# Optimization experiments

Measured on AMD Instinct MI355X. Metric: run time of the kernel, lower is better.

The kernel has to match this reference:

```python
import jax, jax.numpy as jnp
import numpy as np

N = 100_000   # nodes
E = 800_000   # edges
D = 128       # hidden_dim
L = 4         # layer_num
G = 512       # graphs in batch
T = 10        # target_dim
BN_EPS = 1e-5


def setup_inputs() -> dict:
    key = jax.random.key(0)
    ks = jax.random.split(key, 16)
    return {
        "x": jax.random.randint(ks[0], (N, 9), 0, 64),
        "edge_index": jax.random.randint(ks[1], (2, E), 0, N),
        "batch": jnp.sort(jax.random.randint(ks[2], (N,), 0, G)),
        "edge_attr": jax.random.randint(ks[3], (E, 3), 0, 8),
        "atom_emb": jax.random.normal(ks[4], (9, 64, D), jnp.float32) * 0.1,
        "W": jax.random.normal(ks[5], (L, D, D), jnp.float32) * 0.05,
        "b": jax.random.normal(ks[6], (L, D), jnp.float32) * 0.01,
        "root": jax.random.normal(ks[7], (L, D), jnp.float32) * 0.1,
        "bond_emb": jax.random.normal(ks[8], (L, 3, 8, D), jnp.float32) * 0.1,
        "gamma": jnp.ones((L, D), jnp.float32),
        "beta": jnp.zeros((L, D), jnp.float32),
        "W1": jax.random.normal(ks[9], (D, D), jnp.float32) * 0.05,
        "b1": jax.random.normal(ks[10], (D,), jnp.float32) * 0.01,
        "W2": jax.random.normal(ks[11], (D, T), jnp.float32) * 0.05,
        "b2": jax.random.normal(ks[12], (T,), jnp.float32) * 0.01,
    }


def reference(x, edge_index, batch, edge_attr, atom_emb, W, b, root,
              bond_emb, gamma, beta, W1, b1, W2, b2):
    # AtomEncoder: sum of 9 per-feature embeddings -> [N, D]
    h = atom_emb[jnp.arange(9)[None, :], x].sum(axis=1)

    row, col = edge_index[0], edge_index[1]  # source j, target i
    # degree(row, N) + 1 (same every layer)
    deg = jax.ops.segment_sum(jnp.ones((E,), h.dtype), row, num_segments=N) + 1.0
    dinv = deg ** -0.5
    norm = dinv[row] * dinv[col]  # [E]

    feat3 = jnp.arange(3)[None, :]
    for l in range(L):
        hl = h @ W[l] + b[l]                                   # linear
        e = bond_emb[l][feat3, edge_attr].sum(axis=1)          # BondEncoder [E, D]
        msg = norm[:, None] * jax.nn.relu(hl[row] + e)         # gather + message
        aggr = jax.ops.segment_sum(msg, col, num_segments=N)   # scatter-add
        h = aggr + jax.nn.relu(hl + root[l]) / deg[:, None]
        if l < L - 1:
            mu = h.mean(axis=0)
            var = jnp.var(h, axis=0)                           # biased, as torch BN train
            h = (h - mu) / jnp.sqrt(var + BN_EPS) * gamma[l] + beta[l]
            h = jax.nn.relu(h)
        # dropout is identity in eval mode

    # global mean pool over graphs
    counts = jax.ops.segment_sum(jnp.ones((N,), h.dtype), batch, num_segments=G)
    hg = jax.ops.segment_sum(h, batch, num_segments=G) / jnp.maximum(counts, 1.0)[:, None]

    # output MLP: ReLU -> Linear -> ReLU -> Linear
    hh = jax.nn.relu(hg)
    hh = jax.nn.relu(hh @ W1 + b1)
    return hh @ W2 + b2
```

## Files before the change

### kernel.cpp

```cpp
#include <hip/hip_runtime.h>
#include <hip/hip_fp16.h>

#define NN 100000
#define NE 800000
#define DD 128
#define NL 4
#define NG 512
#define NT 10
#define BN_EPS 1e-5f
#define SCAN_B 1024
#define CHUNK 13

typedef __attribute__((ext_vector_type(4))) float f32x4;
typedef __attribute__((ext_vector_type(8))) _Float16 f16x8;

__device__ __forceinline__ float atomAddF(float* p, float v) {
  return unsafeAtomicAdd(p, v);
}


__global__ __launch_bounds__(256) void edge_count_kernel(
    const int* __restrict__ ei, int* __restrict__ degcnt,
    int* __restrict__ incnt) {
  int t = blockIdx.x * 256 + threadIdx.x;
  if (t * 4 >= NE) return;
  int4 s = *reinterpret_cast<const int4*>(&ei[t * 4]);
  int4 d = *reinterpret_cast<const int4*>(&ei[NE + t * 4]);
  atomicAdd(&degcnt[s.x], 1);
  atomicAdd(&degcnt[s.y], 1);
  atomicAdd(&degcnt[s.z], 1);
  atomicAdd(&degcnt[s.w], 1);
  atomicAdd(&incnt[d.x], 1);
  atomicAdd(&incnt[d.y], 1);
  atomicAdd(&incnt[d.z], 1);
  atomicAdd(&incnt[d.w], 1);
}


__global__ __launch_bounds__(256) void tables_kernel(
    const float* __restrict__ W, __half* __restrict__ Wf,
    const float* __restrict__ atom_emb, __half* __restrict__ aemb16,
    const int* __restrict__ batch, int* __restrict__ gstart) {
  const int idx = blockIdx.x * 256 + threadIdx.x;
  if (idx < NL * 8 * 4 * 64) {
    int lane = idx & 63;
    int c = (idx >> 6) & 3;
    int t = (idx >> 8) & 7;
    int l = idx >> 11;
    const float* Wl = W + l * DD * DD;
    __half* o = Wf + idx * 8;
    int n = t * 16 + (lane & 15);
    int k0 = c * 32 + (lane >> 4) * 8;
#pragma unroll
    for (int i = 0; i < 8; ++i) o[i] = (__half)Wl[(k0 + i) * DD + n];
  }
  if (idx < 9 * 64 * 32) {
    float4 v = *reinterpret_cast<const float4*>(&atom_emb[idx * 4]);
    union { __half2 hh[2]; int2 i2; } u;
    u.hh[0] = __floats2half2_rn(v.x, v.y);
    u.hh[1] = __floats2half2_rn(v.z, v.w);
    *reinterpret_cast<int2*>(&aemb16[idx * 4]) = u.i2;
  }
  if (idx <= NG) {
    if (idx == NG) {
      gstart[NG] = NN;
    } else {
      int lo = 0, hi = NN;
      while (lo < hi) {
        int m = (lo + hi) >> 1;
        if (batch[m] < idx) lo = m + 1; else hi = m;
      }
      gstart[idx] = lo;
    }
  }
}


__global__ __launch_bounds__(256) void atom_encoder_kernel(
    const int* __restrict__ x, const __half* __restrict__ aemb16,
    __half* __restrict__ h) {
  __shared__ int xs[16 * 9];
  const int nb = blockIdx.x * 16;
  const int t = threadIdx.x;
  if (t < 144) {
    int gi = nb * 9 + t;
    xs[t] = (gi < NN * 9) ? x[gi] : 0;
  }
  __syncthreads();
  const int n = nb + (t >> 4);
  const int q8 = t & 15;
  if (n >= NN) return;
  const f16x8* av = reinterpret_cast<const f16x8*>(aemb16);
  float acc[8] = {};
#pragma unroll
  for (int f = 0; f < 9; ++f) {
    int r = xs[(t >> 4) * 9 + f];
    f16x8 v = av[(f * 64 + r) * 16 + q8];
#pragma unroll
    for (int i = 0; i < 8; ++i) acc[i] += (float)v[i];
  }
  union { __half2 hh[4]; int4 i4; } u;
#pragma unroll
  for (int i = 0; i < 4; ++i)
    u.hh[i] = __floats2half2_rn(acc[2 * i], acc[2 * i + 1]);
  *reinterpret_cast<int4*>(&h[n * DD + q8 * 8]) = u.i4;
}


__global__ __launch_bounds__(256) void scan1_kernel(
    const int* __restrict__ in, int* __restrict__ out, int* __restrict__ bsum,
    const int* __restrict__ degcnt, float* __restrict__ degrecip,
    float* __restrict__ dinv, int n) {
  __shared__ int s[256];
  int base = blockIdx.x * SCAN_B + threadIdx.x * 4;
  int v[4] = {0, 0, 0, 0};
  if (base + 3 < n) {
    int4 t = *reinterpret_cast<const int4*>(&in[base]);
    v[0] = t.x; v[1] = t.y; v[2] = t.z; v[3] = t.w;
  } else {
    for (int i = 0; i < 4; ++i) v[i] = (base + i < n) ? in[base + i] : 0;
  }
  for (int i = 0; i < 4; ++i) {
    if (base + i < n) {
      float dv = (float)degcnt[base + i] + 1.f;
      degrecip[base + i] = 1.f / dv;
      dinv[base + i] = rsqrtf(dv);
    }
  }
  int tsum = v[0] + v[1] + v[2] + v[3];
  s[threadIdx.x] = tsum;
  __syncthreads();
  for (int d = 1; d < 256; d <<= 1) {
    int t = (threadIdx.x >= d) ? s[threadIdx.x - d] : 0;
    __syncthreads();
    s[threadIdx.x] += t;
    __syncthreads();
  }
  int run = s[threadIdx.x] - tsum;
  if (threadIdx.x == 255) bsum[blockIdx.x] = s[255];
  for (int i = 0; i < 4; ++i) {
    if (base + i < n) out[base + i] = run;
    run += v[i];
  }
}

__global__ void scan2_kernel(int* bsum, int nb) {
  __shared__ int s[128];
  int v = (threadIdx.x < nb) ? bsum[threadIdx.x] : 0;
  s[threadIdx.x] = v;
  __syncthreads();
  for (int d = 1; d < 128; d <<= 1) {
    int t = (threadIdx.x >= d) ? s[threadIdx.x - d] : 0;
    __syncthreads();
    s[threadIdx.x] += t;
    __syncthreads();
  }
  if (threadIdx.x < nb) bsum[threadIdx.x] = s[threadIdx.x] - v;
}

__global__ __launch_bounds__(256) void scan3_kernel(int* off, const int* bsum,
                                                    int n, int total) {
  int i = blockIdx.x * 256 + threadIdx.x;
  if (i < n) off[i] += bsum[i / SCAN_B];
  if (i == 0) off[n] = total;
}

__global__ __launch_bounds__(256) void csr_fill_kernel(
    const int* __restrict__ ei, const int* __restrict__ eattr,
    const float* __restrict__ dinv, const int* __restrict__ off,
    int* __restrict__ cursor, int2* __restrict__ edata) {
  int e = blockIdx.x * 256 + threadIdx.x;
  if (e >= NE) return;
  int r = ei[e], c = ei[NE + e];
  int pos = atomicAdd(&cursor[c], 1);
  float nm = dinv[r] * dinv[c];
  int idx9 = eattr[e * 3] | (eattr[e * 3 + 1] << 3) | (eattr[e * 3 + 2] << 6);
  int2 d;
  d.x = r | (idx9 << 17);
  d.y = __float_as_int(nm);
  edata[off[c] + pos] = d;
}


__global__ __launch_bounds__(256) void gemm_mfma_kernel(
    const __half* __restrict__ A, const __half* __restrict__ Wf,
    const float* __restrict__ bias, const float* __restrict__ bn_scale,
    const float* __restrict__ bn_shift, int fuse_bn, __half* __restrict__ hl) {
  const int wid = threadIdx.x >> 6, lane = threadIdx.x & 63;
  const int r0 = blockIdx.x * 64 + wid * 16;
  const int arow = min(r0 + (lane & 15), NN - 1);
  const int kb = (lane >> 4) * 8;

  f16x8 afrag[4];
#pragma unroll
  for (int c = 0; c < 4; ++c) {
    const int k0 = c * 32 + kb;
    f16x8 raw = *reinterpret_cast<const f16x8*>(&A[arow * DD + k0]);
    if (fuse_bn) {
#pragma unroll
      for (int i = 0; i < 8; ++i) {
        float v = fmaxf((float)raw[i] * bn_scale[k0 + i] + bn_shift[k0 + i], 0.f);
        raw[i] = (_Float16)v;
      }
    }
    afrag[c] = raw;
  }

  f32x4 acc[8];
#pragma unroll
  for (int t = 0; t < 8; ++t) acc[t] = (f32x4){0.f, 0.f, 0.f, 0.f};

  const f16x8* __restrict__ wf = reinterpret_cast<const f16x8*>(Wf);
#pragma unroll
  for (int t = 0; t < 8; ++t) {
#pragma unroll
    for (int c = 0; c < 4; ++c) {
      f16x8 b = wf[(t * 4 + c) * 64 + lane];
      acc[t] = __builtin_amdgcn_mfma_f32_16x16x32_f16(afrag[c], b, acc[t], 0, 0, 0);
    }
  }

  const int colb = lane & 15;
  const int rbase = r0 + (lane >> 4) * 4;
#pragma unroll
  for (int t = 0; t < 8; ++t) {
    float bb = bias[t * 16 + colb];
#pragma unroll
    for (int j = 0; j < 4; ++j) {
      int row = rbase + j;
      if (row < NN) hl[row * DD + t * 16 + colb] = (__half)(acc[t][j] + bb);
    }
  }
}


#define PROC(E)                                                   \
  {                                                               \
    int p_ = (E).x;                                               \
    float nm_ = __int_as_float((E).y);                            \
    float2 hv_ = __half22float2(hl2[(p_ & 0x1FFFF) * 64 + lane]); \
    int i9_ = p_ >> 17;                                           \
    float2 b0_ = bembS[(i9_ & 7) * 64 + lane];                    \
    float2 b1_ = bembS[(8 + ((i9_ >> 3) & 7)) * 64 + lane];       \
    float2 b2_ = bembS[(16 + ((i9_ >> 6) & 7)) * 64 + lane];      \
    acc0 += nm_ * fmaxf(hv_.x + b0_.x + b1_.x + b2_.x, 0.f);      \
    acc1 += nm_ * fmaxf(hv_.y + b0_.y + b1_.y + b2_.y, 0.f);      \
  }

__global__ __launch_bounds__(256) void gather_update_kernel(
    const int* __restrict__ off, const int2* __restrict__ edata,
    const __half2* __restrict__ hl2, const float* __restrict__ bemb,
    const float* __restrict__ root, const float* __restrict__ degrecip,
    const int* __restrict__ batch, __half2* __restrict__ h2,
    float* __restrict__ hg, float* __restrict__ bn_sum,
    float* __restrict__ bn_sq, int mode) {
  __shared__ float2 bembS[24 * 64];
  const float2* bemb2 = reinterpret_cast<const float2*>(bemb);
  for (int i = threadIdx.x; i < 24 * 64; i += 256) bembS[i] = bemb2[i];
  const int wid = threadIdx.x >> 6;
  const int lane = threadIdx.x & 63;
  float2 rt = *reinterpret_cast<const float2*>(&root[2 * lane]);
  float ls0 = 0, ls1 = 0, lq0 = 0, lq1 = 0;
  const int wv = blockIdx.x * 4 + wid;
  const int n0 = wv * CHUNK;
  const int n1 = min(n0 + CHUNK, NN);
  int curg = -1;
  float pg0 = 0.f, pg1 = 0.f;
  __syncthreads();
  for (int n = n0; n < n1; ++n) {
    int k0 = off[n], k1 = off[n + 1];
    float acc0 = 0.f, acc1 = 0.f;
    int k = k0;
    for (; k + 3 < k1; k += 4) {
      int2 e0 = edata[k], e1 = edata[k + 1], e2 = edata[k + 2],
           e3 = edata[k + 3];
      PROC(e0) PROC(e1) PROC(e2) PROC(e3)
    }
    for (; k < k1; ++k) {
      int2 e0 = edata[k];
      PROC(e0)
    }
    float dr = degrecip[n];
    float2 hs = __half22float2(hl2[n * 64 + lane]);
    float v0 = acc0 + fmaxf(hs.x + rt.x, 0.f) * dr;
    float v1 = acc1 + fmaxf(hs.y + rt.y, 0.f) * dr;
    if (mode == 0) {
      h2[n * 64 + lane] = __floats2half2_rn(v0, v1);
      ls0 += v0; ls1 += v1;
      lq0 += v0 * v0; lq1 += v1 * v1;
    } else {
      int g = batch[n];
      if (g != curg) {
        if (curg >= 0) {
          atomAddF(&hg[curg * DD + 2 * lane], pg0);
          atomAddF(&hg[curg * DD + 2 * lane + 1], pg1);
        }
        curg = g;
        pg0 = v0; pg1 = v1;
      } else {
        pg0 += v0; pg1 += v1;
      }
    }
  }
  if (mode == 1) {
    if (curg >= 0) {
      atomAddF(&hg[curg * DD + 2 * lane], pg0);
      atomAddF(&hg[curg * DD + 2 * lane + 1], pg1);
    }
    return;
  }
  __shared__ float s0[DD], s1[DD];
  const int d0 = 2 * lane, d1 = 2 * lane + 1;
  if (wid == 0) {
    s0[d0] = ls0; s0[d1] = ls1;
    s1[d0] = lq0; s1[d1] = lq1;
  }
  __syncthreads();
#pragma unroll
  for (int w = 1; w < 4; ++w) {
    if (wid == w) {
      s0[d0] += ls0; s0[d1] += ls1;
      s1[d0] += lq0; s1[d1] += lq1;
    }
    __syncthreads();
  }
  if (threadIdx.x < DD) {
    atomAddF(&bn_sum[threadIdx.x], s0[threadIdx.x]);
    atomAddF(&bn_sq[threadIdx.x], s1[threadIdx.x]);
  }
}

__global__ __launch_bounds__(128) void bn_finalize_kernel(
    const float* __restrict__ bn_sum, const float* __restrict__ bn_sq,
    const float* __restrict__ gamma, const float* __restrict__ beta,
    float* __restrict__ scale, float* __restrict__ shift) {
  int d = threadIdx.x;
  float mu = bn_sum[d] / (float)NN;
  float var = bn_sq[d] / (float)NN - mu * mu;
  float inv = rsqrtf(var + BN_EPS);
  float sc = gamma[d] * inv;
  scale[d] = sc;
  shift[d] = beta[d] - mu * sc;
}


__global__ __launch_bounds__(128) void mlp_kernel(
    const float* __restrict__ hg, const int* __restrict__ gstart,
    const float* __restrict__ W1, const float* __restrict__ b1,
    const float* __restrict__ W2, const float* __restrict__ b2,
    float* __restrict__ out) {
  int g = blockIdx.x, t = threadIdx.x;
  float cnt = fmaxf((float)(gstart[g + 1] - gstart[g]), 1.f);
  __shared__ float row[DD], t1[DD];
  row[t] = fmaxf(hg[g * DD + t] / cnt, 0.f);
  __syncthreads();
  float a1v = b1[t];
  for (int k = 0; k < DD; ++k) a1v = fmaf(row[k], W1[k * DD + t], a1v);
  t1[t] = fmaxf(a1v, 0.f);
  __syncthreads();
  if (t < NT) {
    float a2 = b2[t];
    for (int k = 0; k < DD; ++k) a2 = fmaf(t1[k], W2[k * NT + t], a2);
    out[g * NT + t] = a2;
  }
}

extern "C" void kernel_launch(void* const* d_in, const int* in_sizes, int n_in,
                              void* d_out, int out_size, void* d_ws,
                              size_t ws_size, hipStream_t stream) {
  const int* x = (const int*)d_in[0];
  const int* edge_index = (const int*)d_in[1];
  const int* batch = (const int*)d_in[2];
  const int* edge_attr = (const int*)d_in[3];
  const float* atom_emb = (const float*)d_in[4];
  const float* W = (const float*)d_in[5];
  const float* b = (const float*)d_in[6];
  const float* root = (const float*)d_in[7];
  const float* bond_emb = (const float*)d_in[8];
  const float* gamma = (const float*)d_in[9];
  const float* beta = (const float*)d_in[10];
  const float* W1 = (const float*)d_in[11];
  const float* b1 = (const float*)d_in[12];
  const float* W2 = (const float*)d_in[13];
  const float* b2 = (const float*)d_in[14];
  float* out = (float*)d_out;

  char* ws = (char*)d_ws;
  size_t off_b = 0;
  auto alloc = [&](size_t bytes) {
    char* p = ws + off_b;
    off_b += (bytes + 255) & ~size_t(255);
    return p;
  };
  __half* h = (__half*)alloc(sizeof(__half) * NN * DD);
  __half* hl = (__half*)alloc(sizeof(__half) * NN * DD);
  int2* edata = (int2*)alloc(sizeof(int2) * NE);
  float* degrecip = (float*)alloc(sizeof(float) * NN);
  float* dinv = (float*)alloc(sizeof(float) * NN);
  int* off = (int*)alloc(sizeof(int) * (NN + 1));
  int* bsum = (int*)alloc(sizeof(int) * 128);
  float* bsc = (float*)alloc(sizeof(float) * DD);
  float* bsh = (float*)alloc(sizeof(float) * DD);
  int* gstart = (int*)alloc(sizeof(int) * (NG + 1));
  __half* Wf = (__half*)alloc(sizeof(__half) * NL * DD * DD);
  __half* aemb16 = (__half*)alloc(sizeof(__half) * 9 * 64 * DD);
  char* zstart = ws + off_b;
  int* degcnt = (int*)alloc(sizeof(int) * NN);
  int* incnt = (int*)alloc(sizeof(int) * NN);
  int* cursor = (int*)alloc(sizeof(int) * NN);
  float* hg = (float*)alloc(sizeof(float) * NG * DD);
  float* bnS = (float*)alloc(sizeof(float) * NL * DD);
  float* bnQ = (float*)alloc(sizeof(float) * NL * DD);
  size_t zbytes = (ws + off_b) - zstart;

  hipMemsetAsync(zstart, 0, zbytes, stream);

  edge_count_kernel<<<(NE / 4 + 255) / 256, 256, 0, stream>>>(edge_index,
                                                              degcnt, incnt);
  tables_kernel<<<(9 * 64 * 32 + 255) / 256, 256, 0, stream>>>(
      W, Wf, atom_emb, aemb16, batch, gstart);
  atom_encoder_kernel<<<(NN * 16 + 255) / 256, 256, 0, stream>>>(x, aemb16, h);

  const int nb = (NN + SCAN_B - 1) / SCAN_B;
  scan1_kernel<<<nb, 256, 0, stream>>>(incnt, off, bsum, degcnt, degrecip,
                                       dinv, NN);
  scan2_kernel<<<1, 128, 0, stream>>>(bsum, nb);
  scan3_kernel<<<(NN + 255) / 256, 256, 0, stream>>>(off, bsum, NN, NE);
  csr_fill_kernel<<<(NE + 255) / 256, 256, 0, stream>>>(edge_index, edge_attr,
                                                        dinv, off, cursor, edata);

  const int GB = (NN + 4 * CHUNK - 1) / (4 * CHUNK);
  for (int l = 0; l < NL; ++l) {
    gemm_mfma_kernel<<<(NN + 63) / 64, 256, 0, stream>>>(
        h, Wf + l * DD * DD, b + l * DD, bsc, bsh, l > 0 ? 1 : 0, hl);
    int mode = (l < NL - 1) ? 0 : 1;
    gather_update_kernel<<<GB, 256, 0, stream>>>(
        off, edata, (const __half2*)hl, bond_emb + l * 3 * 8 * DD,
        root + l * DD, degrecip, batch, (__half2*)h, hg, bnS + l * DD,
        bnQ + l * DD, mode);
    if (mode == 0) {
      bn_finalize_kernel<<<1, DD, 0, stream>>>(bnS + l * DD, bnQ + l * DD,
                                               gamma + l * DD, beta + l * DD,
                                               bsc, bsh);
    }
  }

  mlp_kernel<<<NG, DD, 0, stream>>>(hg, gstart, W1, b1, W2, b2, out);
}
```

Baseline: 578.7 us.

## Record in-edge ranks during counting, store bond table as half, shrink chunk size

```diff
diff --git a/kernel.cpp b/kernel.cpp
--- a/kernel.cpp
+++ b/kernel.cpp
@@ -9,7 +9,7 @@
 #define NT 10
 #define BN_EPS 1e-5f
 #define SCAN_B 1024
-#define CHUNK 13
+#define CHUNK 7
 
 typedef __attribute__((ext_vector_type(4))) float f32x4;
 typedef __attribute__((ext_vector_type(8))) _Float16 f16x8;
@@ -21,7 +21,7 @@
 
 __global__ __launch_bounds__(256) void edge_count_kernel(
     const int* __restrict__ ei, int* __restrict__ degcnt,
-    int* __restrict__ incnt) {
+    int* __restrict__ incnt, int* __restrict__ erank) {
   int t = blockIdx.x * 256 + threadIdx.x;
   if (t * 4 >= NE) return;
   int4 s = *reinterpret_cast<const int4*>(&ei[t * 4]);
@@ -30,10 +30,12 @@
   atomicAdd(&degcnt[s.y], 1);
   atomicAdd(&degcnt[s.z], 1);
   atomicAdd(&degcnt[s.w], 1);
-  atomicAdd(&incnt[d.x], 1);
-  atomicAdd(&incnt[d.y], 1);
-  atomicAdd(&incnt[d.z], 1);
-  atomicAdd(&incnt[d.w], 1);
+  int4 r;
+  r.x = atomicAdd(&incnt[d.x], 1);
+  r.y = atomicAdd(&incnt[d.y], 1);
+  r.z = atomicAdd(&incnt[d.z], 1);
+  r.w = atomicAdd(&incnt[d.w], 1);
+  *reinterpret_cast<int4*>(&erank[t * 4]) = r;
 }
 
 
@@ -168,17 +170,17 @@
 __global__ __launch_bounds__(256) void csr_fill_kernel(
     const int* __restrict__ ei, const int* __restrict__ eattr,
     const float* __restrict__ dinv, const int* __restrict__ off,
-    int* __restrict__ cursor, int2* __restrict__ edata) {
+    const int* __restrict__ erank, int2* __restrict__ edata) {
   int e = blockIdx.x * 256 + threadIdx.x;
   if (e >= NE) return;
   int r = ei[e], c = ei[NE + e];
-  int pos = atomicAdd(&cursor[c], 1);
+  int pos = off[c] + erank[e];
   float nm = dinv[r] * dinv[c];
   int idx9 = eattr[e * 3] | (eattr[e * 3 + 1] << 3) | (eattr[e * 3 + 2] << 6);
   int2 d;
   d.x = r | (idx9 << 17);
   d.y = __float_as_int(nm);
-  edata[off[c] + pos] = d;
+  edata[pos] = d;
 }
 
 
@@ -234,17 +236,17 @@
 }
 
 
-#define PROC(E)                                                   \
-  {                                                               \
-    int p_ = (E).x;                                               \
-    float nm_ = __int_as_float((E).y);                            \
-    float2 hv_ = __half22float2(hl2[(p_ & 0x1FFFF) * 64 + lane]); \
-    int i9_ = p_ >> 17;                                           \
-    float2 b0_ = bembS[(i9_ & 7) * 64 + lane];                    \
-    float2 b1_ = bembS[(8 + ((i9_ >> 3) & 7)) * 64 + lane];       \
-    float2 b2_ = bembS[(16 + ((i9_ >> 6) & 7)) * 64 + lane];      \
-    acc0 += nm_ * fmaxf(hv_.x + b0_.x + b1_.x + b2_.x, 0.f);      \
-    acc1 += nm_ * fmaxf(hv_.y + b0_.y + b1_.y + b2_.y, 0.f);      \
+#define PROC(E)                                                       \
+  {                                                                   \
+    int p_ = (E).x;                                                   \
+    float nm_ = __int_as_float((E).y);                                \
+    float2 hv_ = __half22float2(hl2[(p_ & 0x1FFFF) * 64 + lane]);     \
+    int i9_ = p_ >> 17;                                               \
+    float2 b0_ = __half22float2(bembS[(i9_ & 7) * 64 + lane]);        \
+    float2 b1_ = __half22float2(bembS[(8 + ((i9_ >> 3) & 7)) * 64 + lane]); \
+    float2 b2_ = __half22float2(bembS[(16 + ((i9_ >> 6) & 7)) * 64 + lane]); \
+    acc0 += nm_ * fmaxf(hv_.x + b0_.x + b1_.x + b2_.x, 0.f);          \
+    acc1 += nm_ * fmaxf(hv_.y + b0_.y + b1_.y + b2_.y, 0.f);          \
   }
 
 __global__ __launch_bounds__(256) void gather_update_kernel(
@@ -254,9 +256,12 @@
     const int* __restrict__ batch, __half2* __restrict__ h2,
     float* __restrict__ hg, float* __restrict__ bn_sum,
     float* __restrict__ bn_sq, int mode) {
-  __shared__ float2 bembS[24 * 64];
+  __shared__ __half2 bembS[24 * 64];
   const float2* bemb2 = reinterpret_cast<const float2*>(bemb);
-  for (int i = threadIdx.x; i < 24 * 64; i += 256) bembS[i] = bemb2[i];
+  for (int i = threadIdx.x; i < 24 * 64; i += 256) {
+    float2 v = bemb2[i];
+    bembS[i] = __floats2half2_rn(v.x, v.y);
+  }
   const int wid = threadIdx.x >> 6;
   const int lane = threadIdx.x & 63;
   float2 rt = *reinterpret_cast<const float2*>(&root[2 * lane]);
@@ -395,6 +400,7 @@
   __half* h = (__half*)alloc(sizeof(__half) * NN * DD);
   __half* hl = (__half*)alloc(sizeof(__half) * NN * DD);
   int2* edata = (int2*)alloc(sizeof(int2) * NE);
+  int* erank = (int*)alloc(sizeof(int) * NE);
   float* degrecip = (float*)alloc(sizeof(float) * NN);
   float* dinv = (float*)alloc(sizeof(float) * NN);
   int* off = (int*)alloc(sizeof(int) * (NN + 1));
@@ -407,7 +413,6 @@
   char* zstart = ws + off_b;
   int* degcnt = (int*)alloc(sizeof(int) * NN);
   int* incnt = (int*)alloc(sizeof(int) * NN);
-  int* cursor = (int*)alloc(sizeof(int) * NN);
   float* hg = (float*)alloc(sizeof(float) * NG * DD);
   float* bnS = (float*)alloc(sizeof(float) * NL * DD);
   float* bnQ = (float*)alloc(sizeof(float) * NL * DD);
@@ -415,8 +420,8 @@
 
   hipMemsetAsync(zstart, 0, zbytes, stream);
 
-  edge_count_kernel<<<(NE / 4 + 255) / 256, 256, 0, stream>>>(edge_index,
-                                                              degcnt, incnt);
+  edge_count_kernel<<<(NE / 4 + 255) / 256, 256, 0, stream>>>(
+      edge_index, degcnt, incnt, erank);
   tables_kernel<<<(9 * 64 * 32 + 255) / 256, 256, 0, stream>>>(
       W, Wf, atom_emb, aemb16, batch, gstart);
   atom_encoder_kernel<<<(NN * 16 + 255) / 256, 256, 0, stream>>>(x, aemb16, h);
@@ -427,7 +432,7 @@
   scan2_kernel<<<1, 128, 0, stream>>>(bsum, nb);
   scan3_kernel<<<(NN + 255) / 256, 256, 0, stream>>>(off, bsum, NN, NE);
   csr_fill_kernel<<<(NE + 255) / 256, 256, 0, stream>>>(edge_index, edge_attr,
-                                                        dinv, off, cursor, edata);
+                                                        dinv, off, erank, edata);
 
   const int GB = (NN + 4 * CHUNK - 1) / (4 * CHUNK);
   for (int l = 0; l < NL; ++l) {
```

Result: slower. 666.1 us (+15.1%).
